# Kernel optimization log

Hardware: AMD Instinct MI355X
Metric: run time of the kernel (lower is better)

## Reference

```python
import jax, jax.numpy as jnp
import numpy as np

NQ, NK, D, DV = 8192, 2048, 2048, 2048

def setup_inputs() -> dict:
    key = jax.random.key(0)
    kq, kk, kv, km = jax.random.split(key, 4)
    Query = jax.random.normal(kq, (NQ, D), dtype=jnp.float32)
    Key = jax.random.normal(kk, (NK, D), dtype=jnp.float32)
    Value = jax.random.normal(kv, (NK, DV), dtype=jnp.float32)
    # binary multiplicative mask (keep prob 0.5); row-all-zero has negligible probability at NK=2048
    mask = (jax.random.uniform(km, (NQ, NK)) > 0.5).astype(jnp.float32)
    return {"Query": Query, "Key": Key, "Value": Value, "mask": mask}

def reference(Query, Key, Value, mask):
    d = Key.shape[1]
    scale = 1.0 / jnp.sqrt(jnp.asarray(d, dtype=Query.dtype))
    scores = jnp.einsum('qd,kd->qk', Query, Key) * scale  # [Nq, Nk]
    energy = jax.nn.softmax(scores, axis=-1) * mask
    att = energy / jnp.sum(energy, axis=-1, keepdims=True)  # renormalize after mask
    return jnp.einsum('qk,kv->qv', att, Value)
```

## Files before the change

kernel.cpp:

```cpp
#include <hip/hip_runtime.h>
#include <hip/hip_bf16.h>


#define NQ 8192
#define NK 2048
#define DD 2048
#define DVV 2048

typedef __attribute__((ext_vector_type(8))) short short8;
typedef __attribute__((ext_vector_type(4))) float f32x4;

typedef __attribute__((address_space(3))) void as3_void;
typedef __attribute__((address_space(1))) const void as1_cvoid;
#define GLOAD16(g, l) __builtin_amdgcn_global_load_lds((as1_cvoid*)(g), (as3_void*)(l), 16, 0, 0)

#define SBAR do { __builtin_amdgcn_sched_barrier(0); __builtin_amdgcn_s_barrier(); } while (0)
#define WLG0 do { asm volatile("s_waitcnt lgkmcnt(0)" ::: "memory"); __builtin_amdgcn_sched_barrier(0); } while (0)

__device__ inline float bf2f(short s) {
    union { unsigned u; float f; } x;
    x.u = ((unsigned)(unsigned short)s) << 16;
    return x.f;
}

__global__ __launch_bounds__(256) void conv_bf16_kernel(
    __hip_bfloat16* __restrict__ dst, const float* __restrict__ src, int n4)
{
    int stride = gridDim.x * blockDim.x;
    for (int i = blockIdx.x * blockDim.x + threadIdx.x; i < n4; i += stride) {
        float4 f = reinterpret_cast<const float4*>(src)[i];
        union { __hip_bfloat16 h[4]; uint2 u; } p;
        p.h[0] = __float2bfloat16(f.x);
        p.h[1] = __float2bfloat16(f.y);
        p.h[2] = __float2bfloat16(f.z);
        p.h[3] = __float2bfloat16(f.w);
        reinterpret_cast<uint2*>(dst)[i] = p.u;
    }
}

__global__ __launch_bounds__(256) void transpose_conv_kernel(
    __hip_bfloat16* __restrict__ Vt, const float* __restrict__ V)
{
    __shared__ __hip_bfloat16 tile[64][65];
    const int tx = threadIdx.x;
    const int ty = threadIdx.y;
    const int r0 = blockIdx.y * 64;
    const int c0 = blockIdx.x * 64;
    #pragma unroll
    for (int j = ty; j < 64; j += 4)
        tile[j][tx] = __float2bfloat16(V[(size_t)(r0 + j) * DVV + c0 + tx]);
    __syncthreads();
    #pragma unroll
    for (int j = ty; j < 64; j += 4)
        Vt[(size_t)(c0 + j) * NK + r0 + tx] = tile[tx][j];
}

template<int EPI>
__global__ __launch_bounds__(512, 2) void gemm_nt8_kernel(
    void* __restrict__ Cv,
    const __hip_bfloat16* __restrict__ A,
    const __hip_bfloat16* __restrict__ B,
    const float* __restrict__ aux,
    int K, int lda, int ldb, int ldc, float scale)
{
    constexpr int BM = 256, BN = 256, BK = 64;
    const int NT = K / BK;
    __shared__ __align__(16) __hip_bfloat16 As[2][BM * BK];
    __shared__ __align__(16) __hip_bfloat16 Bs[2][BN * BK];

    const int tid  = threadIdx.x;
    const int wave = tid >> 6;
    const int lane = tid & 63;
    const int wm   = wave >> 2;
    const int wn   = wave & 3;
    const int fr   = lane & 15;
    const int fq   = lane >> 4;

    const int swz = (blockIdx.x & 7) * 32 + (blockIdx.x >> 3);
    const int bm  = swz >> 3;
    const int bn  = swz & 7;

    const int srow = tid >> 3;
    const int scol = (((tid & 7) ^ (srow & 7)) << 3);

    const __hip_bfloat16* Ab = A + (size_t)(bm * BM) * lda;
    const __hip_bfloat16* Bb = B + (size_t)(bn * BN) * ldb;

    f32x4 acc[8][4];
    #pragma unroll
    for (int i = 0; i < 8; ++i)
        #pragma unroll
        for (int j = 0; j < 4; ++j)
            acc[i][j] = (f32x4){0.f, 0.f, 0.f, 0.f};

    short8 af[4][2], b0[2][2], b1[2][2];

    auto stage_a = [&](int pp, int h, int kt) {
        GLOAD16(Ab + (size_t)(h * 128 +      srow) * lda + kt + scol,
                &As[pp][(h * 1024 +       wave * 64) * 8]);
        GLOAD16(Ab + (size_t)(h * 128 + 64 + srow) * lda + kt + scol,
                &As[pp][(h * 1024 + 512 + wave * 64) * 8]);
    };
    auto stage_b = [&](int pp, int h, int kt) {
        GLOAD16(Bb + (size_t)(h * 128 +      srow) * ldb + kt + scol,
                &Bs[pp][(h * 1024 +       wave * 64) * 8]);
        GLOAD16(Bb + (size_t)(h * 128 + 64 + srow) * ldb + kt + scol,
                &Bs[pp][(h * 1024 + 512 + wave * 64) * 8]);
    };
    auto load_a = [&](int pp, int mh) {
        #pragma unroll
        for (int mi = 0; mi < 4; ++mi)
            #pragma unroll
            for (int kk = 0; kk < 2; ++kk) {
                const int row = mh * 128 + wm * 64 + mi * 16 + fr;
                af[mi][kk] = *(const short8*)
                    &As[pp][row * 64 + ((((kk << 2) | fq) ^ (fr & 7)) << 3)];
            }
    };
    auto load_b = [&](int pp, int nh, short8 (&dst)[2][2]) {
        #pragma unroll
        for (int ni = 0; ni < 2; ++ni)
            #pragma unroll
            for (int kk = 0; kk < 2; ++kk) {
                const int row = nh * 128 + wn * 32 + ni * 16 + fr;
                dst[ni][kk] = *(const short8*)
                    &Bs[pp][row * 64 + ((((kk << 2) | fq) ^ (fr & 7)) << 3)];
            }
    };

#define QUAD(mh, nh, bset) do {                                              \
        __builtin_amdgcn_s_setprio(1);                                       \
        _Pragma("unroll")                                                    \
        for (int mi = 0; mi < 4; ++mi)                                       \
            _Pragma("unroll")                                                \
            for (int ni = 0; ni < 2; ++ni)                                   \
                _Pragma("unroll")                                            \
                for (int kk = 0; kk < 2; ++kk)                               \
                    acc[(mh) * 4 + mi][(nh) * 2 + ni] =                      \
                        __builtin_amdgcn_mfma_f32_16x16x32_bf16(             \
                            af[mi][kk], bset[ni][kk],                        \
                            acc[(mh) * 4 + mi][(nh) * 2 + ni], 0, 0, 0);     \
        __builtin_amdgcn_s_setprio(0);                                       \
    } while (0)

    stage_a(0, 0, 0); stage_b(0, 0, 0);
    stage_a(0, 1, 0); stage_b(0, 1, 0);
    if (NT > 1) {
        stage_a(1, 0, BK); stage_b(1, 0, BK);
        asm volatile("s_waitcnt vmcnt(4)" ::: "memory");
    } else {
        asm volatile("s_waitcnt vmcnt(0)" ::: "memory");
    }
    SBAR;

    for (int t = 0; t < NT; ++t) {
        const int p  = t & 1;
        const int q  = p ^ 1;
        const int k1 = (t + 1) * BK;
        const int k2 = (t + 2) * BK;
        load_a(p, 0);
        load_b(p, 0, b0);
        if (t + 1 < NT) stage_a(q, 1, k1);
        SBAR; WLG0;
        QUAD(0, 0, b0);
        SBAR;
        load_b(p, 1, b1);
        if (t + 1 < NT) stage_b(q, 1, k1);
        SBAR; WLG0;
        QUAD(0, 1, b1);
        SBAR;
        load_a(p, 1);
        if (t + 2 < NT) stage_a(p, 0, k2);
        SBAR; WLG0;
        QUAD(1, 0, b0);
        SBAR;
        if (t + 2 < NT) stage_b(p, 0, k2);
        SBAR;
        QUAD(1, 1, b1);
        if (t + 2 < NT) { asm volatile("s_waitcnt vmcnt(4)" ::: "memory"); }
        else            { asm volatile("s_waitcnt vmcnt(0)" ::: "memory"); }
        SBAR;
    }
#undef QUAD

    #pragma unroll
    for (int mi = 0; mi < 8; ++mi) {
        const int row = bm * BM + (mi >> 2) * 128 + wm * 64 + (mi & 3) * 16 + fq * 4;
        if constexpr (EPI == 1) {
            __hip_bfloat16* C = (__hip_bfloat16*)Cv;
            #pragma unroll
            for (int ni = 0; ni < 4; ++ni) {
                const int col = bn * BN + (ni >> 1) * 128 + wn * 32 + (ni & 1) * 16 + fr;
                #pragma unroll
                for (int r = 0; r < 4; ++r) {
                    const size_t idx = (size_t)(row + r) * ldc + col;
                    float e = __expf(acc[mi][ni][r] * scale) * aux[idx];
                    C[idx] = __float2bfloat16(e);
                }
            }
        } else {
            float* C = (float*)Cv;
            float iv[4];
            #pragma unroll
            for (int r = 0; r < 4; ++r) iv[r] = aux[row + r];
            #pragma unroll
            for (int ni = 0; ni < 4; ++ni) {
                const int col = bn * BN + (ni >> 1) * 128 + wn * 32 + (ni & 1) * 16 + fr;
                #pragma unroll
                for (int r = 0; r < 4; ++r)
                    C[(size_t)(row + r) * ldc + col] = acc[mi][ni][r] * iv[r];
            }
        }
    }
}

__global__ __launch_bounds__(256) void rowinv_kernel(
    float* __restrict__ rowinv, const __hip_bfloat16* __restrict__ P)
{
    const int q    = blockIdx.x;
    const int t    = threadIdx.x;
    const int wave = t >> 6;
    const int lane = t & 63;

    const short8 v = reinterpret_cast<const short8*>(P + (size_t)q * NK)[t];
    float s = 0.f;
    #pragma unroll
    for (int j = 0; j < 8; ++j) s += bf2f(v[j]);
    #pragma unroll
    for (int off = 32; off > 0; off >>= 1)
        s += __shfl_xor(s, off);

    __shared__ float red[4];
    if (lane == 0) red[wave] = s;
    __syncthreads();
    if (t == 0)
        rowinv[q] = 1.0f / ((red[0] + red[1]) + (red[2] + red[3]));
}

extern "C" void kernel_launch(void* const* d_in, const int* in_sizes, int n_in,
                              void* d_out, int out_size, void* d_ws, size_t ws_size,
                              hipStream_t stream)
{
    const float* Q    = (const float*)d_in[0];
    const float* Km   = (const float*)d_in[1];
    const float* V    = (const float*)d_in[2];
    const float* mask = (const float*)d_in[3];
    float* out = (float*)d_out;

    char* ws = (char*)d_ws;
    __hip_bfloat16* Qb  = (__hip_bfloat16*)ws;
    __hip_bfloat16* Kb  = (__hip_bfloat16*)(ws + (size_t)32 * 1024 * 1024);
    __hip_bfloat16* Vtb = (__hip_bfloat16*)(ws + (size_t)40 * 1024 * 1024);
    __hip_bfloat16* P   = (__hip_bfloat16*)(ws + (size_t)48 * 1024 * 1024);
    float*       rowinv = (float*)        (ws + (size_t)80 * 1024 * 1024);

    conv_bf16_kernel<<<2048, 256, 0, stream>>>(Qb, Q, NQ * DD / 4);
    conv_bf16_kernel<<<1024, 256, 0, stream>>>(Kb, Km, NK * DD / 4);
    transpose_conv_kernel<<<dim3(DVV / 64, NK / 64), dim3(64, 4), 0, stream>>>(Vtb, V);

    const float scale = 0.022097086912079608f;
    gemm_nt8_kernel<1><<<256, 512, 0, stream>>>(P, Qb, Kb, mask, DD, DD, DD, NK, scale);
    rowinv_kernel<<<NQ, 256, 0, stream>>>(rowinv, P);
    gemm_nt8_kernel<2><<<256, 512, 0, stream>>>(out, P, Vtb, rowinv,
                                                NK, NK, NK, DVV, 1.0f);
}
```

Measured before the change: 331.8 us.

## Fuse masked row-sum into first GEMM epilogue and drop rowinv kernel

The first GEMM epilogue now accumulates each row's sum of masked exponentials and reduces it across lanes with shuffles. It then adds the partial sums into a zeroed global rowsum buffer using atomics. The second GEMM takes the reciprocal on load. This removes the separate rowinv kernel, which re-read the whole bf16 P matrix, at the cost of a memset and some atomic traffic. The explicit lgkmcnt(0) waits before each MFMA quad are also removed, leaving LDS wait placement to the compiler.

```diff
diff --git a/kernel.cpp b/kernel.cpp
--- a/kernel.cpp
+++ b/kernel.cpp
@@ -15,13 +15,6 @@
 #define GLOAD16(g, l) __builtin_amdgcn_global_load_lds((as1_cvoid*)(g), (as3_void*)(l), 16, 0, 0)
 
 #define SBAR do { __builtin_amdgcn_sched_barrier(0); __builtin_amdgcn_s_barrier(); } while (0)
-#define WLG0 do { asm volatile("s_waitcnt lgkmcnt(0)" ::: "memory"); __builtin_amdgcn_sched_barrier(0); } while (0)
-
-__device__ inline float bf2f(short s) {
-    union { unsigned u; float f; } x;
-    x.u = ((unsigned)(unsigned short)s) << 16;
-    return x.f;
-}
 
 __global__ __launch_bounds__(256) void conv_bf16_kernel(
     __hip_bfloat16* __restrict__ dst, const float* __restrict__ src, int n4)
@@ -61,6 +54,7 @@
     const __hip_bfloat16* __restrict__ A,
     const __hip_bfloat16* __restrict__ B,
     const float* __restrict__ aux,
+    float* __restrict__ rs,
     int K, int lda, int ldb, int ldc, float scale)
 {
     constexpr int BM = 256, BN = 256, BK = 64;
@@ -161,17 +155,17 @@
         load_a(p, 0);
         load_b(p, 0, b0);
         if (t + 1 < NT) stage_a(q, 1, k1);
-        SBAR; WLG0;
+        SBAR;
         QUAD(0, 0, b0);
         SBAR;
         load_b(p, 1, b1);
         if (t + 1 < NT) stage_b(q, 1, k1);
-        SBAR; WLG0;
+        SBAR;
         QUAD(0, 1, b1);
         SBAR;
         load_a(p, 1);
         if (t + 2 < NT) stage_a(p, 0, k2);
-        SBAR; WLG0;
+        SBAR;
         QUAD(1, 0, b0);
         SBAR;
         if (t + 2 < NT) stage_b(p, 0, k2);
@@ -188,6 +182,7 @@
         const int row = bm * BM + (mi >> 2) * 128 + wm * 64 + (mi & 3) * 16 + fq * 4;
         if constexpr (EPI == 1) {
             __hip_bfloat16* C = (__hip_bfloat16*)Cv;
+            float rsum[4] = {0.f, 0.f, 0.f, 0.f};
             #pragma unroll
             for (int ni = 0; ni < 4; ++ni) {
                 const int col = bn * BN + (ni >> 1) * 128 + wn * 32 + (ni & 1) * 16 + fr;
@@ -196,13 +191,23 @@
                     const size_t idx = (size_t)(row + r) * ldc + col;
                     float e = __expf(acc[mi][ni][r] * scale) * aux[idx];
                     C[idx] = __float2bfloat16(e);
+                    rsum[r] += e;
                 }
+            }
+            #pragma unroll
+            for (int r = 0; r < 4; ++r) {
+                float s = rsum[r];
+                s += __shfl_xor(s, 1);
+                s += __shfl_xor(s, 2);
+                s += __shfl_xor(s, 4);
+                s += __shfl_xor(s, 8);
+                if (fr == 0) atomicAdd(&rs[row + r], s);
             }
         } else {
             float* C = (float*)Cv;
             float iv[4];
             #pragma unroll
-            for (int r = 0; r < 4; ++r) iv[r] = aux[row + r];
+            for (int r = 0; r < 4; ++r) iv[r] = 1.0f / aux[row + r];
             #pragma unroll
             for (int ni = 0; ni < 4; ++ni) {
                 const int col = bn * BN + (ni >> 1) * 128 + wn * 32 + (ni & 1) * 16 + fr;
@@ -214,29 +219,6 @@
     }
 }
 
-__global__ __launch_bounds__(256) void rowinv_kernel(
-    float* __restrict__ rowinv, const __hip_bfloat16* __restrict__ P)
-{
-    const int q    = blockIdx.x;
-    const int t    = threadIdx.x;
-    const int wave = t >> 6;
-    const int lane = t & 63;
-
-    const short8 v = reinterpret_cast<const short8*>(P + (size_t)q * NK)[t];
-    float s = 0.f;
-    #pragma unroll
-    for (int j = 0; j < 8; ++j) s += bf2f(v[j]);
-    #pragma unroll
-    for (int off = 32; off > 0; off >>= 1)
-        s += __shfl_xor(s, off);
-
-    __shared__ float red[4];
-    if (lane == 0) red[wave] = s;
-    __syncthreads();
-    if (t == 0)
-        rowinv[q] = 1.0f / ((red[0] + red[1]) + (red[2] + red[3]));
-}
-
 extern "C" void kernel_launch(void* const* d_in, const int* in_sizes, int n_in,
                               void* d_out, int out_size, void* d_ws, size_t ws_size,
                               hipStream_t stream)
@@ -252,15 +234,16 @@
     __hip_bfloat16* Kb  = (__hip_bfloat16*)(ws + (size_t)32 * 1024 * 1024);
     __hip_bfloat16* Vtb = (__hip_bfloat16*)(ws + (size_t)40 * 1024 * 1024);
     __hip_bfloat16* P   = (__hip_bfloat16*)(ws + (size_t)48 * 1024 * 1024);
-    float*       rowinv = (float*)        (ws + (size_t)80 * 1024 * 1024);
+    float*       rowsum = (float*)        (ws + (size_t)80 * 1024 * 1024);
 
     conv_bf16_kernel<<<2048, 256, 0, stream>>>(Qb, Q, NQ * DD / 4);
     conv_bf16_kernel<<<1024, 256, 0, stream>>>(Kb, Km, NK * DD / 4);
     transpose_conv_kernel<<<dim3(DVV / 64, NK / 64), dim3(64, 4), 0, stream>>>(Vtb, V);
+    hipMemsetAsync(rowsum, 0, NQ * sizeof(float), stream);
 
     const float scale = 0.022097086912079608f;
-    gemm_nt8_kernel<1><<<256, 512, 0, stream>>>(P, Qb, Kb, mask, DD, DD, DD, NK, scale);
-    rowinv_kernel<<<NQ, 256, 0, stream>>>(rowinv, P);
-    gemm_nt8_kernel<2><<<256, 512, 0, stream>>>(out, P, Vtb, rowinv,
+    gemm_nt8_kernel<1><<<256, 512, 0, stream>>>(P, Qb, Kb, mask, rowsum,
+                                                DD, DD, DD, NK, scale);
+    gemm_nt8_kernel<2><<<256, 512, 0, stream>>>(out, P, Vtb, rowsum, nullptr,
                                                 NK, NK, NK, DVV, 1.0f);
 }
```

Result: no change. 327.1 us (-1.4%).
